# Performance work log

Hardware: AMD Instinct MI355X
Metric: run time of the kernel (lower is better)

The kernel has to match this reference:

```python
import jax, jax.numpy as jnp
import numpy as np

N = 20000      # atoms
E = 320000     # edges
F = 128        # node_size (hard-pinned by split(128) / expand to 384)
RBF = 20
RC = 5.0
ITERS = 3
NM = 64        # molecules in batch


def setup_inputs() -> dict:
    key = jax.random.key(0)
    ks = iter(jax.random.split(key, 64))
    def nrm(shape, scale=0.05):
        return jax.random.normal(next(ks), shape, dtype=jnp.float32) * scale
    inp = {}
    inp["z"] = jax.random.randint(next(ks), (N,), 0, 119)
    inp["graph"] = jax.random.randint(next(ks), (E, 2), 0, N)
    inp["edges_dist"] = jax.random.uniform(next(ks), (E,), minval=0.5, maxval=RC, dtype=jnp.float32)
    sense = jax.random.normal(next(ks), (E, 3), dtype=jnp.float32)
    inp["edges_sense"] = sense / jnp.linalg.norm(sense, axis=1, keepdims=True)
    inp["graph_idx"] = jnp.sort(jax.random.randint(next(ks), (N,), 0, NM))
    # parameters (stacked over ITERS message/update blocks)
    inp["emb"] = nrm((119, F), 1.0)
    inp["mw1"] = nrm((ITERS, F, F)); inp["mb1"] = nrm((ITERS, F))
    inp["mw2"] = nrm((ITERS, 3 * F, F)); inp["mb2"] = nrm((ITERS, 3 * F))
    inp["ew"] = nrm((ITERS, 3 * F, RBF)); inp["eb"] = nrm((ITERS, 3 * F))
    inp["uw"] = nrm((ITERS, F, F)); inp["vw"] = nrm((ITERS, F, F))
    inp["aw1"] = nrm((ITERS, F, 2 * F)); inp["ab1"] = nrm((ITERS, F))
    inp["aw2"] = nrm((ITERS, 3 * F, F)); inp["ab2"] = nrm((ITERS, 3 * F))
    inp["ow1"] = nrm((F, F)); inp["ob1"] = nrm((F,))
    inp["ow2"] = nrm((1, F)); inp["ob2"] = nrm((1,))
    return inp


def reference(z, graph, edges_dist, edges_sense, graph_idx,
              emb, mw1, mb1, mw2, mb2, ew, eb,
              uw, vw, aw1, ab1, aw2, ab2, ow1, ob1, ow2, ob2):
    src = graph[:, 0]   # scatter target (index_add index)
    dst = graph[:, 1]   # gather source (neighbour)
    s = emb[z]                                  # [N, F]
    v = jnp.zeros((N, 3, F), dtype=s.dtype)     # [N, 3, F]
    # edge-level precompute (same every iteration)
    n = jnp.arange(1, RBF + 1, dtype=jnp.float32)
    d = edges_dist[:, None]
    rbf = jnp.sin(n * jnp.pi * d / RC) / d                              # [E, RBF]
    cut = 0.5 * (jnp.cos(jnp.pi * edges_dist / RC) + 1.0) * (edges_dist < RC)  # [E]
    for i in range(ITERS):
        # --- Message block ---
        a = jax.nn.silu(s @ mw1[i].T + mb1[i]) @ mw2[i].T + mb2[i]      # [N, 3F]
        dist_rep = (rbf @ ew[i].T + eb[i]) * cut[:, None]               # [E, 3F]
        res = a[dst] * dist_rep                                         # [E, 3F]
        rv, rs, rd = res[:, :F], res[:, F:2 * F], res[:, 2 * F:]
        resv = v[dst] * rv[:, None, :] + edges_sense[:, :, None] * rd[:, None, :]  # [E,3,F]
        s = s + 2.0 * jax.ops.segment_sum(rs, src, num_segments=N)
        v = v + 2.0 * jax.ops.segment_sum(resv, src, num_segments=N)
        # --- Update block ---
        Uv = v @ uw[i].T                                                # [N,3,F]
        Vv = v @ vw[i].T
        h = jnp.concatenate([s, jnp.linalg.norm(Vv, axis=1)], axis=-1)  # [N, 2F]
        a2 = jax.nn.silu(h @ aw1[i].T + ab1[i]) @ aw2[i].T + ab2[i]     # [N, 3F]
        avv, asv, ass = a2[:, :F], a2[:, F:2 * F], a2[:, 2 * F:]
        s = s + ass + asv * jnp.sum(Uv * Vv, axis=1)
        v = v + avv[:, None, :] * Uv
    out = jax.nn.silu(s @ ow1.T + ob1) @ ow2.T + ob2                    # [N, 1]
    return jax.ops.segment_sum(out, graph_idx, num_segments=NM)         # [NM, 1]
```

## Files before the change

kernel.cpp:

```cpp
#include <hip/hip_runtime.h>
#include <math.h>

#define NN 20000
#define NE 320000
#define FD 128
#define RBFN 20
#define RC_ 5.0f
#define NITER 3
#define NMOL 64
#define F3 384
#define F2 256
#define PI_ 3.14159265358979323846f
#define KB 128
#define LPAD 8
#define SDS 392

typedef __attribute__((ext_vector_type(8))) short  bf16x8;
typedef __attribute__((ext_vector_type(4))) float  floatx4;
typedef unsigned short u16;
typedef unsigned int   u32;

__device__ __forceinline__ u16 f2b(float x) {
    union { float f; unsigned int u; } v; v.f = x;
    unsigned int u = v.u;
    return (u16)((u + 0x7fffu + ((u >> 16) & 1u)) >> 16);
}
__device__ __forceinline__ float b2f(u16 x) {
    union { unsigned int u; float f; } v; v.u = ((unsigned int)x) << 16;
    return v.f;
}
__device__ __forceinline__ float blo(u32 w) {
    union { unsigned int u; float f; } v; v.u = w << 16; return v.f;
}
__device__ __forceinline__ float bhi(u32 w) {
    union { unsigned int u; float f; } v; v.u = w & 0xffff0000u; return v.f;
}
__device__ __forceinline__ u32 pack2(float a, float b) {
    return (u32)f2b(a) | ((u32)f2b(b) << 16);
}

__global__ __launch_bounds__(256) void init_all_kernel(
    const float* s0, int n0, const float* s1, int n1, const float* s2, int n2,
    const float* s3, int n3, const float* s4, int n4, const float* s5, int n5,
    const float* s6, int n6, u16* __restrict__ wdst,
    const float* __restrict__ ew, u16* __restrict__ ewb,
    const int* __restrict__ z, const float* __restrict__ emb,
    float* __restrict__ s, u16* __restrict__ sbf,
    float* __restrict__ v_a, int* __restrict__ v_pk_i, int* __restrict__ cnt)
{
    int idx = blockIdx.x * 256 + threadIdx.x;
    if (idx < NN * F3) v_a[idx] = 0.f;
    if (idx < NN * F3 / 2) v_pk_i[idx] = 0;
    if (idx < NN) cnt[idx] = 0;
    if (idx < NN * FD) {
        int n = idx >> 7, f = idx & 127;
        float v = emb[z[n] * FD + f];
        s[idx] = v; sbf[idx] = f2b(v);
    }
    if (idx < NITER * F3 * 32) {
        int k = idx & 31;
        int row = idx >> 5;
        ewb[idx] = (k < RBFN) ? f2b(ew[row * RBFN + k]) : (u16)0;
    }
    {
        int w = idx;
        u16* dst = wdst;
        if (w < n0) { dst[w] = f2b(s0[w]); return; } w -= n0; dst += n0;
        if (w < n1) { dst[w] = f2b(s1[w]); return; } w -= n1; dst += n1;
        if (w < n2) { dst[w] = f2b(s2[w]); return; } w -= n2; dst += n2;
        if (w < n3) { dst[w] = f2b(s3[w]); return; } w -= n3; dst += n3;
        if (w < n4) { dst[w] = f2b(s4[w]); return; } w -= n4; dst += n4;
        if (w < n5) { dst[w] = f2b(s5[w]); return; } w -= n5; dst += n5;
        if (w < n6) { dst[w] = f2b(s6[w]); }
    }
}

__global__ __launch_bounds__(256) void csr_count_kernel(const int* __restrict__ graph,
    int* __restrict__ cnt)
{
    int e = blockIdx.x * 256 + threadIdx.x;
    if (e >= NE) return;
    atomicAdd(&cnt[graph[2 * e]], 1);
}

__global__ __launch_bounds__(1024) void csr_scan_kernel(const int* __restrict__ cnt,
    int* __restrict__ row_ptr, int* __restrict__ cursor)
{
    __shared__ int sd[1024];
    int tid = threadIdx.x;
    const int chunk = (NN + 1023) / 1024;
    int start = tid * chunk;
    int end = start + chunk; if (end > NN) end = NN;
    int sum = 0;
    for (int j = start; j < end; j++) sum += cnt[j];
    sd[tid] = sum;
    __syncthreads();
    for (int off = 1; off < 1024; off <<= 1) {
        int v = 0;
        if (tid >= off) v = sd[tid - off];
        __syncthreads();
        if (tid >= off) sd[tid] += v;
        __syncthreads();
    }
    int run = (tid == 0) ? 0 : sd[tid - 1];
    for (int j = start; j < end; j++) {
        row_ptr[j] = run;
        cursor[j]  = run;
        run += cnt[j];
    }
    if (tid == 0) row_ptr[NN] = NE;
}

__global__ __launch_bounds__(256) void csr_scatter_kernel(const int* __restrict__ graph,
    int* __restrict__ cursor, int* __restrict__ edge_list)
{
    int e = blockIdx.x * 256 + threadIdx.x;
    if (e >= NE) return;
    int p = atomicAdd(&cursor[graph[2 * e]], 1);
    edge_list[p] = e;
}

__global__ __launch_bounds__(256) void edge_stream_kernel(
    const int* __restrict__ edge_list, const int* __restrict__ graph,
    const float* __restrict__ dist, const float* __restrict__ sense,
    u16* __restrict__ rbf_bf, float* __restrict__ cut_p,
    float* __restrict__ sense_p, int* __restrict__ dst_p)
{
    int j = blockIdx.x * 256 + threadIdx.x;
    if (j >= NE) return;
    int e = edge_list[j];
    float d = dist[e];
    float inv = 1.f / d;
    float base = PI_ * d / RC_;
    float s1, c1;
    __sincosf(base, &s1, &c1);
    float twoc = c1 + c1;
    u16* rb = rbf_bf + (size_t)j * 32;
    float sprev = 0.f, scur = s1;
    #pragma unroll
    for (int k = 0; k < RBFN; k++) {
        rb[k] = f2b(scur * inv);
        float snext = twoc * scur - sprev;
        sprev = scur; scur = snext;
    }
    #pragma unroll
    for (int k = RBFN; k < 32; k++) rb[k] = 0;
    cut_p[j] = 0.5f * (c1 + 1.f) * (d < RC_ ? 1.f : 0.f);
    dst_p[j] = graph[2 * e + 1];
    sense_p[3 * j + 0] = sense[3 * e + 0];
    sense_p[3 * j + 1] = sense[3 * e + 1];
    sense_p[3 * j + 2] = sense[3 * e + 2];
}

template<int K1, bool PACK>
__global__ __launch_bounds__(256) void mlp_kernel(const u16* __restrict__ A,
    const u16* __restrict__ W1, const float* __restrict__ b1,
    const u16* __restrict__ W2, const float* __restrict__ b2,
    u16* __restrict__ Ob, int M)
{
    __shared__ u16 As[64][KB + LPAD];
    __shared__ u16 Ws[128][KB + LPAD];
    __shared__ u16 T[64][KB + LPAD];
    const int bm = blockIdx.x * 64;
    const int tid = threadIdx.x;
    const int wave = tid >> 6, lane = tid & 63;
    const int wm  = (wave >> 1) * 32;
    const int wn1 = (wave & 1) * 64;
    const int wn  = (wave & 1) * 32;
    const int quad = lane >> 4, lr = lane & 15;
    const int r = tid >> 2, q = tid & 3;

    floatx4 acc1[2][4];
    #pragma unroll
    for (int i = 0; i < 2; i++)
        #pragma unroll
        for (int j = 0; j < 4; j++) acc1[i][j] = (floatx4)0.f;

    for (int ko = 0; ko < K1; ko += KB) {
        {
            int gm = bm + r;
            u16* dA = &As[r][q * 32];
            if (gm < M) {
                const u16* ap = A + (size_t)gm * K1 + ko + q * 32;
                #pragma unroll
                for (int x = 0; x < 32; x += 8)
                    *(bf16x8*)&dA[x] = *(const bf16x8*)(ap + x);
            } else {
                #pragma unroll
                for (int x = 0; x < 32; x += 8)
                    *(bf16x8*)&dA[x] = (bf16x8)0;
            }
            #pragma unroll
            for (int h = 0; h < 2; h++) {
                int wr = r + h * 64;
                const u16* wp = W1 + (size_t)wr * K1 + ko + q * 32;
                u16* dW = &Ws[wr][q * 32];
                #pragma unroll
                for (int x = 0; x < 32; x += 8)
                    *(bf16x8*)&dW[x] = *(const bf16x8*)(wp + x);
            }
        }
        __syncthreads();
        #pragma unroll
        for (int kk = 0; kk < KB; kk += 32) {
            bf16x8 a0 = *(const bf16x8*)&As[wm + lr     ][kk + quad * 8];
            bf16x8 a1 = *(const bf16x8*)&As[wm + 16 + lr][kk + quad * 8];
            #pragma unroll
            for (int j = 0; j < 4; j++) {
                bf16x8 b = *(const bf16x8*)&Ws[wn1 + j * 16 + lr][kk + quad * 8];
                acc1[0][j] = __builtin_amdgcn_mfma_f32_16x16x32_bf16(a0, b, acc1[0][j], 0, 0, 0);
                acc1[1][j] = __builtin_amdgcn_mfma_f32_16x16x32_bf16(a1, b, acc1[1][j], 0, 0, 0);
            }
        }
        __syncthreads();
    }
    #pragma unroll
    for (int i = 0; i < 2; i++) {
        #pragma unroll
        for (int j = 0; j < 4; j++) {
            int col = wn1 + j * 16 + lr;
            float bb = b1[col];
            #pragma unroll
            for (int rr = 0; rr < 4; rr++) {
                int row = wm + i * 16 + quad * 4 + rr;
                float v = acc1[i][j][rr] + bb;
                v = v / (1.f + __expf(-v));
                T[row][col] = f2b(v);
            }
        }
    }
    __syncthreads();

    for (int c0 = 0; c0 < F3; c0 += 64) {
        {
            const u16* wp = W2 + (size_t)(c0 + r) * KB + q * 32;
            u16* dW = &Ws[r][q * 32];
            #pragma unroll
            for (int x = 0; x < 32; x += 8)
                *(bf16x8*)&dW[x] = *(const bf16x8*)(wp + x);
        }
        __syncthreads();
        floatx4 acc2[2][2];
        #pragma unroll
        for (int i = 0; i < 2; i++)
            #pragma unroll
            for (int j = 0; j < 2; j++) acc2[i][j] = (floatx4)0.f;
        #pragma unroll
        for (int kk = 0; kk < KB; kk += 32) {
            bf16x8 a0 = *(const bf16x8*)&T[wm + lr     ][kk + quad * 8];
            bf16x8 a1 = *(const bf16x8*)&T[wm + 16 + lr][kk + quad * 8];
            bf16x8 b0 = *(const bf16x8*)&Ws[wn + lr     ][kk + quad * 8];
            bf16x8 b1 = *(const bf16x8*)&Ws[wn + 16 + lr][kk + quad * 8];
            acc2[0][0] = __builtin_amdgcn_mfma_f32_16x16x32_bf16(a0, b0, acc2[0][0], 0, 0, 0);
            acc2[0][1] = __builtin_amdgcn_mfma_f32_16x16x32_bf16(a0, b1, acc2[0][1], 0, 0, 0);
            acc2[1][0] = __builtin_amdgcn_mfma_f32_16x16x32_bf16(a1, b0, acc2[1][0], 0, 0, 0);
            acc2[1][1] = __builtin_amdgcn_mfma_f32_16x16x32_bf16(a1, b1, acc2[1][1], 0, 0, 0);
        }
        #pragma unroll
        for (int i = 0; i < 2; i++) {
            #pragma unroll
            for (int j = 0; j < 2; j++) {
                int gn = c0 + wn + j * 16 + lr;
                float bb = b2[gn];
                #pragma unroll
                for (int rr = 0; rr < 4; rr++) {
                    int gm = bm + wm + i * 16 + quad * 4 + rr;
                    if (gm < M) {
                        u16 val = f2b(acc2[i][j][rr] + bb);
                        if (PACK) {
                            int off = (gn < 256) ? ((gn & 127) * 2 + (gn >> 7))
                                                 : (256 + (gn & 127));
                            Ob[(size_t)gm * F3 + off] = val;
                        } else {
                            Ob[(size_t)gm * F3 + gn] = val;
                        }
                    }
                }
            }
        }
        __syncthreads();
    }
}

__global__ __launch_bounds__(256) void gemm_uv(const u16* __restrict__ A,
    const u16* __restrict__ Wu, const u16* __restrict__ Wv,
    u16* __restrict__ U, u16* __restrict__ V, int M)
{
    __shared__ u16 As[64][KB + LPAD];
    __shared__ u16 Bu[64][KB + LPAD];
    __shared__ u16 Bv[64][KB + LPAD];
    const int bm = blockIdx.x * 64;
    const int bn = blockIdx.y * 64;
    const int tid = threadIdx.x;
    const int r = tid >> 2;
    const int q = tid & 3;
    const int wave = tid >> 6;
    const int lane = tid & 63;
    const int wm = (wave >> 1) * 32;
    const int wn = (wave & 1) * 32;
    const int quad = lane >> 4;
    const int lr = lane & 15;

    floatx4 au[2][2], av[2][2];
    #pragma unroll
    for (int i = 0; i < 2; i++)
        #pragma unroll
        for (int j = 0; j < 2; j++) { au[i][j] = (floatx4)0.f; av[i][j] = (floatx4)0.f; }

    {
        int gm = bm + r;
        u16* dA = &As[r][q * 32];
        if (gm < M) {
            const u16* ap = A + (size_t)gm * KB + q * 32;
            #pragma unroll
            for (int x = 0; x < 32; x += 8)
                *(bf16x8*)&dA[x] = *(const bf16x8*)(ap + x);
        } else {
            #pragma unroll
            for (int x = 0; x < 32; x += 8)
                *(bf16x8*)&dA[x] = (bf16x8)0;
        }
        int gn = bn + r;
        const u16* up = Wu + (size_t)gn * KB + q * 32;
        const u16* vp = Wv + (size_t)gn * KB + q * 32;
        u16* dU = &Bu[r][q * 32];
        u16* dV = &Bv[r][q * 32];
        #pragma unroll
        for (int x = 0; x < 32; x += 8) {
            *(bf16x8*)&dU[x] = *(const bf16x8*)(up + x);
            *(bf16x8*)&dV[x] = *(const bf16x8*)(vp + x);
        }
    }
    __syncthreads();
    #pragma unroll
    for (int kk = 0; kk < KB; kk += 32) {
        bf16x8 a0 = *(const bf16x8*)&As[wm + lr     ][kk + quad * 8];
        bf16x8 a1 = *(const bf16x8*)&As[wm + 16 + lr][kk + quad * 8];
        bf16x8 u0 = *(const bf16x8*)&Bu[wn + lr     ][kk + quad * 8];
        bf16x8 u1 = *(const bf16x8*)&Bu[wn + 16 + lr][kk + quad * 8];
        bf16x8 v0 = *(const bf16x8*)&Bv[wn + lr     ][kk + quad * 8];
        bf16x8 v1 = *(const bf16x8*)&Bv[wn + 16 + lr][kk + quad * 8];
        au[0][0] = __builtin_amdgcn_mfma_f32_16x16x32_bf16(a0, u0, au[0][0], 0, 0, 0);
        au[0][1] = __builtin_amdgcn_mfma_f32_16x16x32_bf16(a0, u1, au[0][1], 0, 0, 0);
        au[1][0] = __builtin_amdgcn_mfma_f32_16x16x32_bf16(a1, u0, au[1][0], 0, 0, 0);
        au[1][1] = __builtin_amdgcn_mfma_f32_16x16x32_bf16(a1, u1, au[1][1], 0, 0, 0);
        av[0][0] = __builtin_amdgcn_mfma_f32_16x16x32_bf16(a0, v0, av[0][0], 0, 0, 0);
        av[0][1] = __builtin_amdgcn_mfma_f32_16x16x32_bf16(a0, v1, av[0][1], 0, 0, 0);
        av[1][0] = __builtin_amdgcn_mfma_f32_16x16x32_bf16(a1, v0, av[1][0], 0, 0, 0);
        av[1][1] = __builtin_amdgcn_mfma_f32_16x16x32_bf16(a1, v1, av[1][1], 0, 0, 0);
    }
    #pragma unroll
    for (int i = 0; i < 2; i++) {
        #pragma unroll
        for (int j = 0; j < 2; j++) {
            int gn = bn + wn + j * 16 + lr;
            #pragma unroll
            for (int rr = 0; rr < 4; rr++) {
                int gm = bm + wm + i * 16 + quad * 4 + rr;
                if (gm < M) {
                    U[(size_t)gm * FD + gn] = f2b(au[i][j][rr]);
                    V[(size_t)gm * FD + gn] = f2b(av[i][j][rr]);
                }
            }
        }
    }
}

__global__ __launch_bounds__(256) void edge_mfma_kernel(
    const u16* __restrict__ rbf_bf, const float* __restrict__ cut_p,
    const float* __restrict__ sense_p, const int* __restrict__ dst_p,
    const u16* __restrict__ ewb, const float* __restrict__ eb,
    const u16* __restrict__ a_pk, const float* __restrict__ s_in,
    const float* __restrict__ v_in, const u16* __restrict__ v_pk,
    const int* __restrict__ row_ptr,
    float* __restrict__ s_out, u16* __restrict__ s_obf,
    float* __restrict__ v_out, u16* __restrict__ v_obf)
{
    __shared__ u16   sdrep[16 * SDS];
    __shared__ float scut[16];
    __shared__ float ssen[16][4];
    __shared__ int   sdst[16];
    __shared__ float red[4 * 128];

    const int n = blockIdx.x;
    const int tid = threadIdx.x;
    const int wave = tid >> 6;
    const int lane = tid & 63;
    const int quad = lane >> 4;
    const int lr = lane & 15;
    const int f = tid & 127;
    const int half = tid >> 7;

    int beg = row_ptr[n], end = row_ptr[n + 1];
    float accs = 0.f, accv0 = 0.f, accv1 = 0.f, accv2 = 0.f;

    for (int t0 = beg; t0 < end; t0 += 16) {
        int cnt = end - t0; if (cnt > 16) cnt = 16;
        __syncthreads();
        if (tid < 16) {
            scut[tid] = (tid < cnt) ? cut_p[t0 + tid] : 0.f;
            sdst[tid] = (tid < cnt) ? dst_p[t0 + tid] : 0;
        }
        if (tid >= 64 && tid < 64 + 3 * cnt) {
            int x = tid - 64;
            ssen[x / 3][x % 3] = sense_p[3 * t0 + x];
        }
        bf16x8 afrag;
        int ge = t0 + lr;
        if (ge < end) afrag = *(const bf16x8*)&rbf_bf[(size_t)ge * 32 + quad * 8];
        else          afrag = (bf16x8)0;
        floatx4 dacc[6];
        #pragma unroll
        for (int nt = 0; nt < 6; nt++) {
            int nrow = (wave * 6 + nt) * 16 + lr;
            bf16x8 bfrag = *(const bf16x8*)&ewb[(size_t)nrow * 32 + quad * 8];
            dacc[nt] = __builtin_amdgcn_mfma_f32_16x16x32_bf16(afrag, bfrag, (floatx4)0.f, 0, 0, 0);
        }
        __syncthreads();
        #pragma unroll
        for (int nt = 0; nt < 6; nt++) {
            int ncol = (wave * 6 + nt) * 16 + lr;
            float ebn = eb[ncol];
            #pragma unroll
            for (int rr = 0; rr < 4; rr++) {
                int e = quad * 4 + rr;
                sdrep[e * SDS + ncol] = f2b((dacc[nt][rr] + ebn) * scut[e]);
            }
        }
        __syncthreads();
        int nh = cnt - half * 8; if (nh > 8) nh = 8;
        for (int k = 0; k < nh; k++) {
            int e = half * 8 + k;
            int dst = sdst[e];
            const u16* sr = &sdrep[e * SDS];
            float drv = b2f(sr[f]);
            float drs = b2f(sr[FD + f]);
            float drd = b2f(sr[2 * FD + f]);
            const u16* ar = a_pk + (size_t)dst * F3;
            u32 ap = *(const u32*)(ar + f * 2);
            float rv = b2f((u16)(ap & 0xffff)) * drv;
            float rs = b2f((u16)(ap >> 16))    * drs;
            float rd = b2f(ar[256 + f])        * drd;
            accs += rs;
            const u16* vr = v_pk + (size_t)dst * F3;
            u32 vp = *(const u32*)(vr + f * 2);
            accv0 += b2f((u16)(vp & 0xffff)) * rv + ssen[e][0] * rd;
            accv1 += b2f((u16)(vp >> 16))    * rv + ssen[e][1] * rd;
            accv2 += b2f(vr[256 + f])        * rv + ssen[e][2] * rd;
        }
    }
    __syncthreads();
    if (half == 1) {
        red[f] = accs; red[128 + f] = accv0; red[256 + f] = accv1; red[384 + f] = accv2;
    }
    __syncthreads();
    if (half == 0) {
        accs  += red[f];       accv0 += red[128 + f];
        accv1 += red[256 + f]; accv2 += red[384 + f];
        int nb = n * FD + f;
        float so = s_in[nb] + 2.f * accs;
        s_out[nb] = so; s_obf[nb] = f2b(so);
        int vb = n * F3 + f;
        float w0 = v_in[vb]           + 2.f * accv0;
        float w1 = v_in[vb + FD]      + 2.f * accv1;
        float w2 = v_in[vb + 2 * FD]  + 2.f * accv2;
        v_out[vb]          = w0; v_obf[vb]          = f2b(w0);
        v_out[vb + FD]     = w1; v_obf[vb + FD]     = f2b(w1);
        v_out[vb + 2 * FD] = w2; v_obf[vb + 2 * FD] = f2b(w2);
    }
}

template<bool LAST>
__global__ __launch_bounds__(256) void mlp2_update_next_kernel(
    const u16* __restrict__ sbf_mid, const float* __restrict__ s_mid,
    const float* __restrict__ v_mid,
    const u16* __restrict__ Uv, const u16* __restrict__ Vv,
    const u16* __restrict__ W1, const float* __restrict__ b1,
    const u16* __restrict__ W2, const float* __restrict__ b2,
    float* __restrict__ s_out,
    float* __restrict__ v_out, u16* __restrict__ v_pk,
    const u16* __restrict__ N_W1, const float* __restrict__ N_b1,
    const u16* __restrict__ N_W2, const float* __restrict__ N_b2,
    u16* __restrict__ a_pk,
    const u16* __restrict__ H_W1, const float* __restrict__ H_b1,
    const float* __restrict__ ow2, const float* __restrict__ ob2,
    float* __restrict__ nodeval, int M)
{
    __shared__ u16 As[64][KB + LPAD];
    __shared__ u16 Ws[128][KB + LPAD];
    __shared__ u16 T[64][KB + LPAD];
    const int bm = blockIdx.x * 64;
    const int tid = threadIdx.x;
    const int wave = tid >> 6, lane = tid & 63;
    const int wm  = (wave >> 1) * 32;
    const int wn1 = (wave & 1) * 64;
    const int wn  = (wave & 1) * 32;
    const int quad = lane >> 4, lr = lane & 15;
    const int r = tid >> 2, q = tid & 3;

    floatx4 acc1[2][4];
    #pragma unroll
    for (int i = 0; i < 2; i++)
        #pragma unroll
        for (int j = 0; j < 4; j++) acc1[i][j] = (floatx4)0.f;

    {
        int gm = bm + r;
        u16* dA = &As[r][q * 32];
        if (gm < M) {
            const u16* ap = sbf_mid + (size_t)gm * FD + q * 32;
            #pragma unroll
            for (int x = 0; x < 32; x += 8)
                *(bf16x8*)&dA[x] = *(const bf16x8*)(ap + x);
        } else {
            #pragma unroll
            for (int x = 0; x < 32; x += 8)
                *(bf16x8*)&dA[x] = (bf16x8)0;
        }
        #pragma unroll
        for (int h = 0; h < 2; h++) {
            int wr = r + h * 64;
            const u16* wp = W1 + (size_t)wr * F2 + q * 32;
            u16* dW = &Ws[wr][q * 32];
            #pragma unroll
            for (int x = 0; x < 32; x += 8)
                *(bf16x8*)&dW[x] = *(const bf16x8*)(wp + x);
        }
    }
    __syncthreads();
    #pragma unroll
    for (int kk = 0; kk < KB; kk += 32) {
        bf16x8 a0 = *(const bf16x8*)&As[wm + lr     ][kk + quad * 8];
        bf16x8 a1 = *(const bf16x8*)&As[wm + 16 + lr][kk + quad * 8];
        #pragma unroll
        for (int j = 0; j < 4; j++) {
            bf16x8 b = *(const bf16x8*)&Ws[wn1 + j * 16 + lr][kk + quad * 8];
            acc1[0][j] = __builtin_amdgcn_mfma_f32_16x16x32_bf16(a0, b, acc1[0][j], 0, 0, 0);
            acc1[1][j] = __builtin_amdgcn_mfma_f32_16x16x32_bf16(a1, b, acc1[1][j], 0, 0, 0);
        }
    }
    __syncthreads();
    {
        int gm = bm + r;
        u16* dA = &As[r][q * 32];
        if (gm < M) {
            const u16* vvp = Vv + (size_t)gm * F3 + q * 32;
            bf16x8 c0[4], c1[4], c2[4];
            #pragma unroll
            for (int t = 0; t < 4; t++) {
                c0[t] = *(const bf16x8*)(vvp + t * 8);
                c1[t] = *(const bf16x8*)(vvp + FD + t * 8);
                c2[t] = *(const bf16x8*)(vvp + 2 * FD + t * 8);
            }
            #pragma unroll
            for (int t = 0; t < 4; t++) {
                #pragma unroll
                for (int x = 0; x < 8; x++) {
                    float a = b2f((u16)c0[t][x]);
                    float b = b2f((u16)c1[t][x]);
                    float c = b2f((u16)c2[t][x]);
                    dA[t * 8 + x] = f2b(sqrtf(a * a + b * b + c * c));
                }
            }
        } else {
            #pragma unroll
            for (int x = 0; x < 32; x += 8)
                *(bf16x8*)&dA[x] = (bf16x8)0;
        }
        #pragma unroll
        for (int h = 0; h < 2; h++) {
            int wr = r + h * 64;
            const u16* wp = W1 + (size_t)wr * F2 + KB + q * 32;
            u16* dW = &Ws[wr][q * 32];
            #pragma unroll
            for (int x = 0; x < 32; x += 8)
                *(bf16x8*)&dW[x] = *(const bf16x8*)(wp + x);
        }
    }
    __syncthreads();
    #pragma unroll
    for (int kk = 0; kk < KB; kk += 32) {
        bf16x8 a0 = *(const bf16x8*)&As[wm + lr     ][kk + quad * 8];
        bf16x8 a1 = *(const bf16x8*)&As[wm + 16 + lr][kk + quad * 8];
        #pragma unroll
        for (int j = 0; j < 4; j++) {
            bf16x8 b = *(const bf16x8*)&Ws[wn1 + j * 16 + lr][kk + quad * 8];
            acc1[0][j] = __builtin_amdgcn_mfma_f32_16x16x32_bf16(a0, b, acc1[0][j], 0, 0, 0);
            acc1[1][j] = __builtin_amdgcn_mfma_f32_16x16x32_bf16(a1, b, acc1[1][j], 0, 0, 0);
        }
    }
    __syncthreads();
    #pragma unroll
    for (int i = 0; i < 2; i++) {
        #pragma unroll
        for (int j = 0; j < 4; j++) {
            int col = wn1 + j * 16 + lr;
            float bb = b1[col];
            #pragma unroll
            for (int rr = 0; rr < 4; rr++) {
                int row = wm + i * 16 + quad * 4 + rr;
                float v = acc1[i][j][rr] + bb;
                v = v / (1.f + __expf(-v));
                T[row][col] = f2b(v);
            }
        }
    }
    __syncthreads();

    float avvr[2][2][4], asvr[2][2][4];
    #pragma unroll
    for (int part = 0; part < 2; part++) {
        #pragma unroll
        for (int piece = 0; piece < 3; piece++) {
            const int c0 = piece * 128 + part * 64;
            {
                const u16* wp = W2 + (size_t)(c0 + r) * KB + q * 32;
                u16* dW = &Ws[r][q * 32];
                #pragma unroll
                for (int x = 0; x < 32; x += 8)
                    *(bf16x8*)&dW[x] = *(const bf16x8*)(wp + x);
            }
            __syncthreads();
            floatx4 acc2[2][2];
            #pragma unroll
            for (int i = 0; i < 2; i++)
                #pragma unroll
                for (int j = 0; j < 2; j++) acc2[i][j] = (floatx4)0.f;
            #pragma unroll
            for (int kk = 0; kk < KB; kk += 32) {
                bf16x8 a0 = *(const bf16x8*)&T[wm + lr     ][kk + quad * 8];
                bf16x8 a1 = *(const bf16x8*)&T[wm + 16 + lr][kk + quad * 8];
                bf16x8 b0 = *(const bf16x8*)&Ws[wn + lr     ][kk + quad * 8];
                bf16x8 b1 = *(const bf16x8*)&Ws[wn + 16 + lr][kk + quad * 8];
                acc2[0][0] = __builtin_amdgcn_mfma_f32_16x16x32_bf16(a0, b0, acc2[0][0], 0, 0, 0);
                acc2[0][1] = __builtin_amdgcn_mfma_f32_16x16x32_bf16(a0, b1, acc2[0][1], 0, 0, 0);
                acc2[1][0] = __builtin_amdgcn_mfma_f32_16x16x32_bf16(a1, b0, acc2[1][0], 0, 0, 0);
                acc2[1][1] = __builtin_amdgcn_mfma_f32_16x16x32_bf16(a1, b1, acc2[1][1], 0, 0, 0);
            }
            if (piece == 0) {
                #pragma unroll
                for (int i = 0; i < 2; i++)
                    #pragma unroll
                    for (int j = 0; j < 2; j++) {
                        int gn = c0 + wn + j * 16 + lr;
                        float bb = b2[gn];
                        #pragma unroll
                        for (int rr = 0; rr < 4; rr++)
                            avvr[i][j][rr] = acc2[i][j][rr] + bb;
                    }
            } else if (piece == 1) {
                #pragma unroll
                for (int i = 0; i < 2; i++)
                    #pragma unroll
                    for (int j = 0; j < 2; j++) {
                        int gn = c0 + wn + j * 16 + lr;
                        float bb = b2[gn];
                        #pragma unroll
                        for (int rr = 0; rr < 4; rr++)
                            asvr[i][j][rr] = acc2[i][j][rr] + bb;
                    }
            } else {
                #pragma unroll
                for (int i = 0; i < 2; i++) {
                    #pragma unroll
                    for (int j = 0; j < 2; j++) {
                        int gn = c0 + wn + j * 16 + lr;
                        int f  = gn - 256;
                        float bb = b2[gn];
                        #pragma unroll
                        for (int rr = 0; rr < 4; rr++) {
                            int row = wm + i * 16 + quad * 4 + rr;
                            int gm = bm + row;
                            if (gm < M) {
                                float ass = acc2[i][j][rr] + bb;
                                float asv = asvr[i][j][rr];
                                float avv = avvr[i][j][rr];
                                int vb = gm * F3 + f;
                                float u0 = b2f(Uv[vb]);
                                float u1 = b2f(Uv[vb + FD]);
                                float u2 = b2f(Uv[vb + 2 * FD]);
                                float w0 = b2f(Vv[vb]);
                                float w1 = b2f(Vv[vb + FD]);
                                float w2 = b2f(Vv[vb + 2 * FD]);
                                float dot = u0 * w0 + u1 * w1 + u2 * w2;
                                int nb = gm * FD + f;
                                float so = s_mid[nb] + ass + asv * dot;
                                s_out[nb] = so;
                                As[row][f] = f2b(so);
                                float y0 = v_mid[vb]          + avv * u0;
                                float y1 = v_mid[vb + FD]     + avv * u1;
                                float y2 = v_mid[vb + 2 * FD] + avv * u2;
                                v_out[vb]          = y0;
                                v_out[vb + FD]     = y1;
                                v_out[vb + 2 * FD] = y2;
                                char* vpb = (char*)v_pk + (size_t)gm * (2 * F3);
                                *(u32*)(vpb + 4 * f) = pack2(y0, y1);
                                *(u16*)(vpb + 512 + 2 * f) = f2b(y2);
                            } else {
                                As[row][f] = 0;
                            }
                        }
                    }
                }
            }
            __syncthreads();
        }
    }

    if constexpr (!LAST) {
        {
            #pragma unroll
            for (int h = 0; h < 2; h++) {
                int wr = r + h * 64;
                const u16* wp = N_W1 + (size_t)wr * KB + q * 32;
                u16* dW = &Ws[wr][q * 32];
                #pragma unroll
                for (int x = 0; x < 32; x += 8)
                    *(bf16x8*)&dW[x] = *(const bf16x8*)(wp + x);
            }
        }
        __syncthreads();
        #pragma unroll
        for (int i = 0; i < 2; i++)
            #pragma unroll
            for (int j = 0; j < 4; j++) acc1[i][j] = (floatx4)0.f;
        #pragma unroll
        for (int kk = 0; kk < KB; kk += 32) {
            bf16x8 a0 = *(const bf16x8*)&As[wm + lr     ][kk + quad * 8];
            bf16x8 a1 = *(const bf16x8*)&As[wm + 16 + lr][kk + quad * 8];
            #pragma unroll
            for (int j = 0; j < 4; j++) {
                bf16x8 b = *(const bf16x8*)&Ws[wn1 + j * 16 + lr][kk + quad * 8];
                acc1[0][j] = __builtin_amdgcn_mfma_f32_16x16x32_bf16(a0, b, acc1[0][j], 0, 0, 0);
                acc1[1][j] = __builtin_amdgcn_mfma_f32_16x16x32_bf16(a1, b, acc1[1][j], 0, 0, 0);
            }
        }
        __syncthreads();
        #pragma unroll
        for (int i = 0; i < 2; i++) {
            #pragma unroll
            for (int j = 0; j < 4; j++) {
                int col = wn1 + j * 16 + lr;
                float bb = N_b1[col];
                #pragma unroll
                for (int rr = 0; rr < 4; rr++) {
                    int row = wm + i * 16 + quad * 4 + rr;
                    float v = acc1[i][j][rr] + bb;
                    v = v / (1.f + __expf(-v));
                    T[row][col] = f2b(v);
                }
            }
        }
        __syncthreads();
        for (int c0 = 0; c0 < F3; c0 += 64) {
            {
                const u16* wp = N_W2 + (size_t)(c0 + r) * KB + q * 32;
                u16* dW = &Ws[r][q * 32];
                #pragma unroll
                for (int x = 0; x < 32; x += 8)
                    *(bf16x8*)&dW[x] = *(const bf16x8*)(wp + x);
            }
            __syncthreads();
            floatx4 acc2[2][2];
            #pragma unroll
            for (int i = 0; i < 2; i++)
                #pragma unroll
                for (int j = 0; j < 2; j++) acc2[i][j] = (floatx4)0.f;
            #pragma unroll
            for (int kk = 0; kk < KB; kk += 32) {
                bf16x8 a0 = *(const bf16x8*)&T[wm + lr     ][kk + quad * 8];
                bf16x8 a1 = *(const bf16x8*)&T[wm + 16 + lr][kk + quad * 8];
                bf16x8 b0 = *(const bf16x8*)&Ws[wn + lr     ][kk + quad * 8];
                bf16x8 b1 = *(const bf16x8*)&Ws[wn + 16 + lr][kk + quad * 8];
                acc2[0][0] = __builtin_amdgcn_mfma_f32_16x16x32_bf16(a0, b0, acc2[0][0], 0, 0, 0);
                acc2[0][1] = __builtin_amdgcn_mfma_f32_16x16x32_bf16(a0, b1, acc2[0][1], 0, 0, 0);
                acc2[1][0] = __builtin_amdgcn_mfma_f32_16x16x32_bf16(a1, b0, acc2[1][0], 0, 0, 0);
                acc2[1][1] = __builtin_amdgcn_mfma_f32_16x16x32_bf16(a1, b1, acc2[1][1], 0, 0, 0);
            }
            #pragma unroll
            for (int i = 0; i < 2; i++) {
                #pragma unroll
                for (int j = 0; j < 2; j++) {
                    int gn = c0 + wn + j * 16 + lr;
                    float bb = N_b2[gn];
                    #pragma unroll
                    for (int rr = 0; rr < 4; rr++) {
                        int gm = bm + wm + i * 16 + quad * 4 + rr;
                        if (gm < M) {
                            u16 val = f2b(acc2[i][j][rr] + bb);
                            int off = (gn < 256) ? ((gn & 127) * 2 + (gn >> 7))
                                                 : (256 + (gn & 127));
                            a_pk[(size_t)gm * F3 + off] = val;
                        }
                    }
                }
            }
            __syncthreads();
        }
    } else {
        {
            #pragma unroll
            for (int h = 0; h < 2; h++) {
                int wr = r + h * 64;
                const u16* wp = H_W1 + (size_t)wr * KB + q * 32;
                u16* dW = &Ws[wr][q * 32];
                #pragma unroll
                for (int x = 0; x < 32; x += 8)
                    *(bf16x8*)&dW[x] = *(const bf16x8*)(wp + x);
            }
        }
        __syncthreads();
        #pragma unroll
        for (int i = 0; i < 2; i++)
            #pragma unroll
            for (int j = 0; j < 4; j++) acc1[i][j] = (floatx4)0.f;
        #pragma unroll
        for (int kk = 0; kk < KB; kk += 32) {
            bf16x8 a0 = *(const bf16x8*)&As[wm + lr     ][kk + quad * 8];
            bf16x8 a1 = *(const bf16x8*)&As[wm + 16 + lr][kk + quad * 8];
            #pragma unroll
            for (int j = 0; j < 4; j++) {
                bf16x8 b = *(const bf16x8*)&Ws[wn1 + j * 16 + lr][kk + quad * 8];
                acc1[0][j] = __builtin_amdgcn_mfma_f32_16x16x32_bf16(a0, b, acc1[0][j], 0, 0, 0);
                acc1[1][j] = __builtin_amdgcn_mfma_f32_16x16x32_bf16(a1, b, acc1[1][j], 0, 0, 0);
            }
        }
        __syncthreads();
        float* Tf   = (float*)&Ws[0][0];
        float* ow2s = (float*)&As[0][0];
        if (tid < KB) ow2s[tid] = ow2[tid];
        #pragma unroll
        for (int i = 0; i < 2; i++) {
            #pragma unroll
            for (int j = 0; j < 4; j++) {
                int col = wn1 + j * 16 + lr;
                float bb = H_b1[col];
                #pragma unroll
                for (int rr = 0; rr < 4; rr++) {
                    int row = wm + i * 16 + quad * 4 + rr;
                    float v = acc1[i][j][rr] + bb;
                    v = v / (1.f + __expf(-v));
                    Tf[row * 132 + col] = v;
                }
            }
        }
        __syncthreads();
        int nl = tid >> 2, seg = tid & 3;
        float v = 0.f;
        #pragma unroll
        for (int x = 0; x < 32; x++) {
            int col = seg * 32 + x;
            v += Tf[nl * 132 + col] * ow2s[col];
        }
        v += __shfl_down(v, 2);
        v += __shfl_down(v, 1);
        if (seg == 0) {
            int gm = bm + nl;
            if (gm < M) nodeval[gm] = v + ob2[0];
        }
    }
}

__global__ __launch_bounds__(1024) void mol_reduce_kernel(const float* __restrict__ nodeval,
    const int* __restrict__ gidx, float* __restrict__ out)
{
    __shared__ float mol[NMOL];
    int tid = threadIdx.x;
    if (tid < NMOL) mol[tid] = 0.f;
    __syncthreads();
    int cur = -1; float acc = 0.f;
    for (int x = tid; x < NN; x += 1024) {
        int g = gidx[x];
        float v = nodeval[x];
        if (g != cur) {
            if (cur >= 0) atomicAdd(&mol[cur], acc);
            cur = g; acc = v;
        } else acc += v;
    }
    if (cur >= 0) atomicAdd(&mol[cur], acc);
    __syncthreads();
    if (tid < NMOL) out[tid] = mol[tid];
}

extern "C" void kernel_launch(void* const* d_in, const int* in_sizes, int n_in,
                              void* d_out, int out_size, void* d_ws, size_t ws_size,
                              hipStream_t stream)
{
    const int*   z     = (const int*)d_in[0];
    const int*   graph = (const int*)d_in[1];
    const float* dist  = (const float*)d_in[2];
    const float* sense = (const float*)d_in[3];
    const int*   gidx  = (const int*)d_in[4];
    const float* emb   = (const float*)d_in[5];
    const float* mw1   = (const float*)d_in[6];
    const float* mb1   = (const float*)d_in[7];
    const float* mw2   = (const float*)d_in[8];
    const float* mb2   = (const float*)d_in[9];
    const float* ew    = (const float*)d_in[10];
    const float* eb    = (const float*)d_in[11];
    const float* uw    = (const float*)d_in[12];
    const float* vw    = (const float*)d_in[13];
    const float* aw1   = (const float*)d_in[14];
    const float* ab1   = (const float*)d_in[15];
    const float* aw2   = (const float*)d_in[16];
    const float* ab2   = (const float*)d_in[17];
    const float* ow1   = (const float*)d_in[18];
    const float* ob1   = (const float*)d_in[19];
    const float* ow2   = (const float*)d_in[20];
    const float* ob2   = (const float*)d_in[21];
    float* out = (float*)d_out;

    float* W = (float*)d_ws;
    float* s_a    = W; W += (size_t)NN * FD;
    float* s_b    = W; W += (size_t)NN * FD;
    float* v_a    = W; W += (size_t)NN * F3;
    float* v_b    = W; W += (size_t)NN * F3;
    float* cut_p  = W; W += (size_t)NE;
    float* sns_p  = W; W += (size_t)NE * 3;
    float* nodeval= W; W += (size_t)NN;
    u16* U = (u16*)W;
    u16* sbf_a = U; U += (size_t)NN * FD;
    u16* sbf_b = U; U += (size_t)NN * FD;
    u16* vbf_b = U; U += (size_t)NN * F3;
    u16* a_pk  = U; U += (size_t)NN * F3;
    u16* v_pk  = U; U += (size_t)NN * F3;
    u16* h_bf  = U; U += (size_t)NN * F2;
    u16* a2_bf = U; U += (size_t)NN * F3;
    u16* Uv_bf = U; U += (size_t)NN * F3;
    u16* Vv_bf = U; U += (size_t)NN * F3;
    u16* rbf_bf= U; U += (size_t)NE * 32;
    u16* ewb   = U; U += (size_t)NITER * F3 * 32;
    u16* wb    = U; U += 557056;
    int* ip = (int*)U;
    int* row_ptr   = ip; ip += NN + 1;
    int* cnt       = ip; ip += NN;
    int* cursor    = ip; ip += NN;
    int* edge_list = ip; ip += NE;
    int* dst_p     = ip; ip += NE;

    u16* wb_mw1 = wb;
    u16* wb_mw2 = wb + 49152;
    u16* wb_uw  = wb + 196608;
    u16* wb_vw  = wb + 245760;
    u16* wb_aw1 = wb + 294912;
    u16* wb_aw2 = wb + 393216;
    u16* wb_ow1 = wb + 540672;

    const int TB = 256;
    dim3 b256(TB);

    init_all_kernel<<<dim3((NN * F3 + TB - 1) / TB), b256, 0, stream>>>(
        mw1, 49152, mw2, 147456, uw, 49152, vw, 49152, aw1, 98304, aw2, 147456,
        ow1, 16384, wb, ew, ewb, z, emb, s_a, sbf_a, v_a, (int*)v_pk, cnt);
    csr_count_kernel<<<dim3((NE + TB - 1) / TB), b256, 0, stream>>>(graph, cnt);
    csr_scan_kernel<<<dim3(1), dim3(1024), 0, stream>>>(cnt, row_ptr, cursor);
    csr_scatter_kernel<<<dim3((NE + TB - 1) / TB), b256, 0, stream>>>(graph, cursor, edge_list);
    edge_stream_kernel<<<dim3((NE + TB - 1) / TB), b256, 0, stream>>>(
        edge_list, graph, dist, sense, rbf_bf, cut_p, sns_p, dst_p);

    dim3 gM((NN + 63) / 64);
    dim3 gV2((3 * NN + 63) / 64, FD / 64);

    mlp_kernel<128, true><<<gM, b256, 0, stream>>>(sbf_a,
        wb_mw1, mb1, wb_mw2, mb2, a_pk, NN);

    for (int i = 0; i < NITER; i++) {
        edge_mfma_kernel<<<dim3(NN), b256, 0, stream>>>(
            rbf_bf, cut_p, sns_p, dst_p,
            ewb + (size_t)i * F3 * 32, eb + (size_t)i * F3,
            a_pk, s_a, v_a, v_pk, row_ptr, s_b, sbf_b, v_b, vbf_b);
        gemm_uv<<<gV2, b256, 0, stream>>>(vbf_b, wb_uw + (size_t)i * FD * FD,
            wb_vw + (size_t)i * FD * FD, Uv_bf, Vv_bf, 3 * NN);
        if (i < NITER - 1) {
            mlp2_update_next_kernel<false><<<gM, b256, 0, stream>>>(
                sbf_b, s_b, v_b, Uv_bf, Vv_bf,
                wb_aw1 + (size_t)i * FD * F2, ab1 + (size_t)i * FD,
                wb_aw2 + (size_t)i * F3 * FD, ab2 + (size_t)i * F3,
                s_a, v_a, v_pk,
                wb_mw1 + (size_t)(i + 1) * FD * FD, mb1 + (size_t)(i + 1) * FD,
                wb_mw2 + (size_t)(i + 1) * F3 * FD, mb2 + (size_t)(i + 1) * F3, a_pk,
                nullptr, nullptr, nullptr, nullptr, nullptr, NN);
        } else {
            mlp2_update_next_kernel<true><<<gM, b256, 0, stream>>>(
                sbf_b, s_b, v_b, Uv_bf, Vv_bf,
                wb_aw1 + (size_t)i * FD * F2, ab1 + (size_t)i * FD,
                wb_aw2 + (size_t)i * F3 * FD, ab2 + (size_t)i * F3,
                s_a, v_a, v_pk,
                nullptr, nullptr, nullptr, nullptr, nullptr,
                wb_ow1, ob1, ow2, ob2, nodeval, NN);
        }
    }

    mol_reduce_kernel<<<dim3(1), dim3(1024), 0, stream>>>(nodeval, gidx, out);
}
```

Measured before the change: 868.5 us.

## Alias MLP scratch into weight tile, loop N inside gemm_uv, vectorize rbf stores

New measurement: 866.5 us. No clear change (-0.2%).

```diff
diff --git a/kernel.cpp b/kernel.cpp
--- a/kernel.cpp
+++ b/kernel.cpp
@@ -135,16 +135,20 @@
     float s1, c1;
     __sincosf(base, &s1, &c1);
     float twoc = c1 + c1;
-    u16* rb = rbf_bf + (size_t)j * 32;
+    u16 tmp[32];
     float sprev = 0.f, scur = s1;
     #pragma unroll
     for (int k = 0; k < RBFN; k++) {
-        rb[k] = f2b(scur * inv);
+        tmp[k] = f2b(scur * inv);
         float snext = twoc * scur - sprev;
         sprev = scur; scur = snext;
     }
     #pragma unroll
-    for (int k = RBFN; k < 32; k++) rb[k] = 0;
+    for (int k = RBFN; k < 32; k++) tmp[k] = 0;
+    u16* rb = rbf_bf + (size_t)j * 32;
+    #pragma unroll
+    for (int x = 0; x < 32; x += 8)
+        *(bf16x8*)&rb[x] = *(const bf16x8*)&tmp[x];
     cut_p[j] = 0.5f * (c1 + 1.f) * (d < RC_ ? 1.f : 0.f);
     dst_p[j] = graph[2 * e + 1];
     sense_p[3 * j + 0] = sense[3 * e + 0];
@@ -160,7 +164,7 @@
 {
     __shared__ u16 As[64][KB + LPAD];
     __shared__ u16 Ws[128][KB + LPAD];
-    __shared__ u16 T[64][KB + LPAD];
+    u16 (*T)[KB + LPAD] = &Ws[64];
     const int bm = blockIdx.x * 64;
     const int tid = threadIdx.x;
     const int wave = tid >> 6, lane = tid & 63;
@@ -229,7 +233,6 @@
             }
         }
     }
-    __syncthreads();
 
     for (int c0 = 0; c0 < F3; c0 += 64) {
         {
@@ -290,7 +293,6 @@
     __shared__ u16 Bu[64][KB + LPAD];
     __shared__ u16 Bv[64][KB + LPAD];
     const int bm = blockIdx.x * 64;
-    const int bn = blockIdx.y * 64;
     const int tid = threadIdx.x;
     const int r = tid >> 2;
     const int q = tid & 3;
@@ -301,12 +303,6 @@
     const int quad = lane >> 4;
     const int lr = lane & 15;
 
-    floatx4 au[2][2], av[2][2];
-    #pragma unroll
-    for (int i = 0; i < 2; i++)
-        #pragma unroll
-        for (int j = 0; j < 2; j++) { au[i][j] = (floatx4)0.f; av[i][j] = (floatx4)0.f; }
-
     {
         int gm = bm + r;
         u16* dA = &As[r][q * 32];
@@ -320,49 +316,61 @@
             for (int x = 0; x < 32; x += 8)
                 *(bf16x8*)&dA[x] = (bf16x8)0;
         }
-        int gn = bn + r;
-        const u16* up = Wu + (size_t)gn * KB + q * 32;
-        const u16* vp = Wv + (size_t)gn * KB + q * 32;
-        u16* dU = &Bu[r][q * 32];
-        u16* dV = &Bv[r][q * 32];
-        #pragma unroll
-        for (int x = 0; x < 32; x += 8) {
-            *(bf16x8*)&dU[x] = *(const bf16x8*)(up + x);
-            *(bf16x8*)&dV[x] = *(const bf16x8*)(vp + x);
-        }
-    }
-    __syncthreads();
+    }
+
     #pragma unroll
-    for (int kk = 0; kk < KB; kk += 32) {
-        bf16x8 a0 = *(const bf16x8*)&As[wm + lr     ][kk + quad * 8];
-        bf16x8 a1 = *(const bf16x8*)&As[wm + 16 + lr][kk + quad * 8];
-        bf16x8 u0 = *(const bf16x8*)&Bu[wn + lr     ][kk + quad * 8];
-        bf16x8 u1 = *(const bf16x8*)&Bu[wn + 16 + lr][kk + quad * 8];
-        bf16x8 v0 = *(const bf16x8*)&Bv[wn + lr     ][kk + quad * 8];
-        bf16x8 v1 = *(const bf16x8*)&Bv[wn + 16 + lr][kk + quad * 8];
-        au[0][0] = __builtin_amdgcn_mfma_f32_16x16x32_bf16(a0, u0, au[0][0], 0, 0, 0);
-        au[0][1] = __builtin_amdgcn_mfma_f32_16x16x32_bf16(a0, u1, au[0][1], 0, 0, 0);
-        au[1][0] = __builtin_amdgcn_mfma_f32_16x16x32_bf16(a1, u0, au[1][0], 0, 0, 0);
-        au[1][1] = __builtin_amdgcn_mfma_f32_16x16x32_bf16(a1, u1, au[1][1], 0, 0, 0);
-        av[0][0] = __builtin_amdgcn_mfma_f32_16x16x32_bf16(a0, v0, av[0][0], 0, 0, 0);
-        av[0][1] = __builtin_amdgcn_mfma_f32_16x16x32_bf16(a0, v1, av[0][1], 0, 0, 0);
-        av[1][0] = __builtin_amdgcn_mfma_f32_16x16x32_bf16(a1, v0, av[1][0], 0, 0, 0);
-        av[1][1] = __builtin_amdgcn_mfma_f32_16x16x32_bf16(a1, v1, av[1][1], 0, 0, 0);
-    }
-    #pragma unroll
-    for (int i = 0; i < 2; i++) {
-        #pragma unroll
-        for (int j = 0; j < 2; j++) {
-            int gn = bn + wn + j * 16 + lr;
-            #pragma unroll
-            for (int rr = 0; rr < 4; rr++) {
-                int gm = bm + wm + i * 16 + quad * 4 + rr;
-                if (gm < M) {
-                    U[(size_t)gm * FD + gn] = f2b(au[i][j][rr]);
-                    V[(size_t)gm * FD + gn] = f2b(av[i][j][rr]);
+    for (int bn = 0; bn < FD; bn += 64) {
+        {
+            int gn = bn + r;
+            const u16* up = Wu + (size_t)gn * KB + q * 32;
+            const u16* vp = Wv + (size_t)gn * KB + q * 32;
+            u16* dU = &Bu[r][q * 32];
+            u16* dV = &Bv[r][q * 32];
+            #pragma unroll
+            for (int x = 0; x < 32; x += 8) {
+                *(bf16x8*)&dU[x] = *(const bf16x8*)(up + x);
+                *(bf16x8*)&dV[x] = *(const bf16x8*)(vp + x);
+            }
+        }
+        __syncthreads();
+        floatx4 au[2][2], av[2][2];
+        #pragma unroll
+        for (int i = 0; i < 2; i++)
+            #pragma unroll
+            for (int j = 0; j < 2; j++) { au[i][j] = (floatx4)0.f; av[i][j] = (floatx4)0.f; }
+        #pragma unroll
+        for (int kk = 0; kk < KB; kk += 32) {
+            bf16x8 a0 = *(const bf16x8*)&As[wm + lr     ][kk + quad * 8];
+            bf16x8 a1 = *(const bf16x8*)&As[wm + 16 + lr][kk + quad * 8];
+            bf16x8 u0 = *(const bf16x8*)&Bu[wn + lr     ][kk + quad * 8];
+            bf16x8 u1 = *(const bf16x8*)&Bu[wn + 16 + lr][kk + quad * 8];
+            bf16x8 v0 = *(const bf16x8*)&Bv[wn + lr     ][kk + quad * 8];
+            bf16x8 v1 = *(const bf16x8*)&Bv[wn + 16 + lr][kk + quad * 8];
+            au[0][0] = __builtin_amdgcn_mfma_f32_16x16x32_bf16(a0, u0, au[0][0], 0, 0, 0);
+            au[0][1] = __builtin_amdgcn_mfma_f32_16x16x32_bf16(a0, u1, au[0][1], 0, 0, 0);
+            au[1][0] = __builtin_amdgcn_mfma_f32_16x16x32_bf16(a1, u0, au[1][0], 0, 0, 0);
+            au[1][1] = __builtin_amdgcn_mfma_f32_16x16x32_bf16(a1, u1, au[1][1], 0, 0, 0);
+            av[0][0] = __builtin_amdgcn_mfma_f32_16x16x32_bf16(a0, v0, av[0][0], 0, 0, 0);
+            av[0][1] = __builtin_amdgcn_mfma_f32_16x16x32_bf16(a0, v1, av[0][1], 0, 0, 0);
+            av[1][0] = __builtin_amdgcn_mfma_f32_16x16x32_bf16(a1, v0, av[1][0], 0, 0, 0);
+            av[1][1] = __builtin_amdgcn_mfma_f32_16x16x32_bf16(a1, v1, av[1][1], 0, 0, 0);
+        }
+        #pragma unroll
+        for (int i = 0; i < 2; i++) {
+            #pragma unroll
+            for (int j = 0; j < 2; j++) {
+                int gn = bn + wn + j * 16 + lr;
+                #pragma unroll
+                for (int rr = 0; rr < 4; rr++) {
+                    int gm = bm + wm + i * 16 + quad * 4 + rr;
+                    if (gm < M) {
+                        U[(size_t)gm * FD + gn] = f2b(au[i][j][rr]);
+                        V[(size_t)gm * FD + gn] = f2b(av[i][j][rr]);
+                    }
                 }
             }
         }
+        __syncthreads();
     }
 }
 
@@ -488,7 +496,7 @@
 {
     __shared__ u16 As[64][KB + LPAD];
     __shared__ u16 Ws[128][KB + LPAD];
-    __shared__ u16 T[64][KB + LPAD];
+    u16 (*T)[KB + LPAD] = &Ws[64];
     const int bm = blockIdx.x * 64;
     const int tid = threadIdx.x;
     const int wave = tid >> 6, lane = tid & 63;
@@ -605,106 +613,104 @@
             }
         }
     }
-    __syncthreads();
 
     float avvr[2][2][4], asvr[2][2][4];
     #pragma unroll
-    for (int part = 0; part < 2; part++) {
-        #pragma unroll
-        for (int piece = 0; piece < 3; piece++) {
-            const int c0 = piece * 128 + part * 64;
-            {
-                const u16* wp = W2 + (size_t)(c0 + r) * KB + q * 32;
-                u16* dW = &Ws[r][q * 32];
-                #pragma unroll
-                for (int x = 0; x < 32; x += 8)
-                    *(bf16x8*)&dW[x] = *(const bf16x8*)(wp + x);
-            }
-            __syncthreads();
-            floatx4 acc2[2][2];
+    for (int pp = 0; pp < 6; pp++) {
+        const int part  = pp / 3;
+        const int piece = pp % 3;
+        const int c0 = piece * 128 + part * 64;
+        {
+            const u16* wp = W2 + (size_t)(c0 + r) * KB + q * 32;
+            u16* dW = &Ws[r][q * 32];
+            #pragma unroll
+            for (int x = 0; x < 32; x += 8)
+                *(bf16x8*)&dW[x] = *(const bf16x8*)(wp + x);
+        }
+        __syncthreads();
+        floatx4 acc2[2][2];
+        #pragma unroll
+        for (int i = 0; i < 2; i++)
+            #pragma unroll
+            for (int j = 0; j < 2; j++) acc2[i][j] = (floatx4)0.f;
+        #pragma unroll
+        for (int kk = 0; kk < KB; kk += 32) {
+            bf16x8 a0 = *(const bf16x8*)&T[wm + lr     ][kk + quad * 8];
+            bf16x8 a1 = *(const bf16x8*)&T[wm + 16 + lr][kk + quad * 8];
+            bf16x8 b0 = *(const bf16x8*)&Ws[wn + lr     ][kk + quad * 8];
+            bf16x8 b1 = *(const bf16x8*)&Ws[wn + 16 + lr][kk + quad * 8];
+            acc2[0][0] = __builtin_amdgcn_mfma_f32_16x16x32_bf16(a0, b0, acc2[0][0], 0, 0, 0);
+            acc2[0][1] = __builtin_amdgcn_mfma_f32_16x16x32_bf16(a0, b1, acc2[0][1], 0, 0, 0);
+            acc2[1][0] = __builtin_amdgcn_mfma_f32_16x16x32_bf16(a1, b0, acc2[1][0], 0, 0, 0);
+            acc2[1][1] = __builtin_amdgcn_mfma_f32_16x16x32_bf16(a1, b1, acc2[1][1], 0, 0, 0);
+        }
+        if (piece == 0) {
             #pragma unroll
             for (int i = 0; i < 2; i++)
                 #pragma unroll
-                for (int j = 0; j < 2; j++) acc2[i][j] = (floatx4)0.f;
-            #pragma unroll
-            for (int kk = 0; kk < KB; kk += 32) {
-                bf16x8 a0 = *(const bf16x8*)&T[wm + lr     ][kk + quad * 8];
-                bf16x8 a1 = *(const bf16x8*)&T[wm + 16 + lr][kk + quad * 8];
-                bf16x8 b0 = *(const bf16x8*)&Ws[wn + lr     ][kk + quad * 8];
-                bf16x8 b1 = *(const bf16x8*)&Ws[wn + 16 + lr][kk + quad * 8];
-                acc2[0][0] = __builtin_amdgcn_mfma_f32_16x16x32_bf16(a0, b0, acc2[0][0], 0, 0, 0);
-                acc2[0][1] = __builtin_amdgcn_mfma_f32_16x16x32_bf16(a0, b1, acc2[0][1], 0, 0, 0);
-                acc2[1][0] = __builtin_amdgcn_mfma_f32_16x16x32_bf16(a1, b0, acc2[1][0], 0, 0, 0);
-                acc2[1][1] = __builtin_amdgcn_mfma_f32_16x16x32_bf16(a1, b1, acc2[1][1], 0, 0, 0);
-            }
-            if (piece == 0) {
-                #pragma unroll
-                for (int i = 0; i < 2; i++)
+                for (int j = 0; j < 2; j++) {
+                    int gn = c0 + wn + j * 16 + lr;
+                    float bb = b2[gn];
                     #pragma unroll
-                    for (int j = 0; j < 2; j++) {
-                        int gn = c0 + wn + j * 16 + lr;
-                        float bb = b2[gn];
-                        #pragma unroll
-                        for (int rr = 0; rr < 4; rr++)
-                            avvr[i][j][rr] = acc2[i][j][rr] + bb;
-                    }
-            } else if (piece == 1) {
-                #pragma unroll
-                for (int i = 0; i < 2; i++)
+                    for (int rr = 0; rr < 4; rr++)
+                        avvr[i][j][rr] = acc2[i][j][rr] + bb;
+                }
+        } else if (piece == 1) {
+            #pragma unroll
+            for (int i = 0; i < 2; i++)
+                #pragma unroll
+                for (int j = 0; j < 2; j++) {
+                    int gn = c0 + wn + j * 16 + lr;
+                    float bb = b2[gn];
                     #pragma unroll
-                    for (int j = 0; j < 2; j++) {
-                        int gn = c0 + wn + j * 16 + lr;
-                        float bb = b2[gn];
-                        #pragma unroll
-                        for (int rr = 0; rr < 4; rr++)
-                            asvr[i][j][rr] = acc2[i][j][rr] + bb;
-                    }
-            } else {
-                #pragma unroll
-                for (int i = 0; i < 2; i++) {
+                    for (int rr = 0; rr < 4; rr++)
+                        asvr[i][j][rr] = acc2[i][j][rr] + bb;
+                }
+        } else {
+            #pragma unroll
+            for (int i = 0; i < 2; i++) {
+                #pragma unroll
+                for (int j = 0; j < 2; j++) {
+                    int gn = c0 + wn + j * 16 + lr;
+                    int f  = gn - 256;
+                    float bb = b2[gn];
                     #pragma unroll
-                    for (int j = 0; j < 2; j++) {
-                        int gn = c0 + wn + j * 16 + lr;
-                        int f  = gn - 256;
-                        float bb = b2[gn];
-                        #pragma unroll
-                        for (int rr = 0; rr < 4; rr++) {
-                            int row = wm + i * 16 + quad * 4 + rr;
-                            int gm = bm + row;
-                            if (gm < M) {
-                                float ass = acc2[i][j][rr] + bb;
-                                float asv = asvr[i][j][rr];
-                                float avv = avvr[i][j][rr];
-                                int vb = gm * F3 + f;
-                                float u0 = b2f(Uv[vb]);
-                                float u1 = b2f(Uv[vb + FD]);
-                                float u2 = b2f(Uv[vb + 2 * FD]);
-                                float w0 = b2f(Vv[vb]);
-                                float w1 = b2f(Vv[vb + FD]);
-                                float w2 = b2f(Vv[vb + 2 * FD]);
-                                float dot = u0 * w0 + u1 * w1 + u2 * w2;
-                                int nb = gm * FD + f;
-                                float so = s_mid[nb] + ass + asv * dot;
-                                s_out[nb] = so;
-                                As[row][f] = f2b(so);
-                                float y0 = v_mid[vb]          + avv * u0;
-                                float y1 = v_mid[vb + FD]     + avv * u1;
-                                float y2 = v_mid[vb + 2 * FD] + avv * u2;
-                                v_out[vb]          = y0;
-                                v_out[vb + FD]     = y1;
-                                v_out[vb + 2 * FD] = y2;
-                                char* vpb = (char*)v_pk + (size_t)gm * (2 * F3);
-                                *(u32*)(vpb + 4 * f) = pack2(y0, y1);
-                                *(u16*)(vpb + 512 + 2 * f) = f2b(y2);
-                            } else {
-                                As[row][f] = 0;
-                            }
+                    for (int rr = 0; rr < 4; rr++) {
+                        int row = wm + i * 16 + quad * 4 + rr;
+                        int gm = bm + row;
+                        if (gm < M) {
+                            float ass = acc2[i][j][rr] + bb;
+                            float asv = asvr[i][j][rr];
+                            float avv = avvr[i][j][rr];
+                            int vb = gm * F3 + f;
+                            float u0 = b2f(Uv[vb]);
+                            float u1 = b2f(Uv[vb + FD]);
+                            float u2 = b2f(Uv[vb + 2 * FD]);
+                            float w0 = b2f(Vv[vb]);
+                            float w1 = b2f(Vv[vb + FD]);
+                            float w2 = b2f(Vv[vb + 2 * FD]);
+                            float dot = u0 * w0 + u1 * w1 + u2 * w2;
+                            int nb = gm * FD + f;
+                            float so = s_mid[nb] + ass + asv * dot;
+                            s_out[nb] = so;
+                            As[row][f] = f2b(so);
+                            float y0 = v_mid[vb]          + avv * u0;
+                            float y1 = v_mid[vb + FD]     + avv * u1;
+                            float y2 = v_mid[vb + 2 * FD] + avv * u2;
+                            v_out[vb]          = y0;
+                            v_out[vb + FD]     = y1;
+                            v_out[vb + 2 * FD] = y2;
+                            char* vpb = (char*)v_pk + (size_t)gm * (2 * F3);
+                            *(u32*)(vpb + 4 * f) = pack2(y0, y1);
+                            *(u16*)(vpb + 512 + 2 * f) = f2b(y2);
+                        } else {
+                            As[row][f] = 0;
                         }
                     }
                 }
             }
-            __syncthreads();
-        }
+        }
+        __syncthreads();
     }
 
     if constexpr (!LAST) {
@@ -751,8 +757,8 @@
                 }
             }
         }
-        __syncthreads();
-        for (int c0 = 0; c0 < F3; c0 += 64) {
+        for (int pp = 0; pp < 6; pp++) {
+            const int c0 = pp * 64;
             {
                 const u16* wp = N_W2 + (size_t)(c0 + r) * KB + q * 32;
                 u16* dW = &Ws[r][q * 32];
@@ -826,7 +832,6 @@
             }
         }
         __syncthreads();
-        float* Tf   = (float*)&Ws[0][0];
         float* ow2s = (float*)&As[0][0];
         if (tid < KB) ow2s[tid] = ow2[tid];
         #pragma unroll
@@ -840,7 +845,7 @@
                     int row = wm + i * 16 + quad * 4 + rr;
                     float v = acc1[i][j][rr] + bb;
                     v = v / (1.f + __expf(-v));
-                    Tf[row * 132 + col] = v;
+                    T[row][col] = f2b(v);
                 }
             }
         }
@@ -850,7 +855,7 @@
         #pragma unroll
         for (int x = 0; x < 32; x++) {
             int col = seg * 32 + x;
-            v += Tf[nl * 132 + col] * ow2s[col];
+            v += b2f(T[nl][col]) * ow2s[col];
         }
         v += __shfl_down(v, 2);
         v += __shfl_down(v, 1);
@@ -959,7 +964,7 @@
         edge_list, graph, dist, sense, rbf_bf, cut_p, sns_p, dst_p);
 
     dim3 gM((NN + 63) / 64);
-    dim3 gV2((3 * NN + 63) / 64, FD / 64);
+    dim3 gUV((3 * NN + 63) / 64);
 
     mlp_kernel<128, true><<<gM, b256, 0, stream>>>(sbf_a,
         wb_mw1, mb1, wb_mw2, mb2, a_pk, NN);
@@ -969,7 +974,7 @@
             rbf_bf, cut_p, sns_p, dst_p,
             ewb + (size_t)i * F3 * 32, eb + (size_t)i * F3,
             a_pk, s_a, v_a, v_pk, row_ptr, s_b, sbf_b, v_b, vbf_b);
-        gemm_uv<<<gV2, b256, 0, stream>>>(vbf_b, wb_uw + (size_t)i * FD * FD,
+        gemm_uv<<<gUV, b256, 0, stream>>>(vbf_b, wb_uw + (size_t)i * FD * FD,
             wb_vw + (size_t)i * FD * FD, Uv_bf, Vv_bf, 3 * NN);
         if (i < NITER - 1) {
             mlp2_update_next_kernel<false><<<gM, b256, 0, stream>>>(
```
